# Kernel tuning notes

Measured on AMD Instinct MI355X. Metric: run time of the kernel, lower is better.

The kernel has to match this reference:

```python
import jax, jax.numpy as jnp
import numpy as np

B, C, H, W = 16, 512, 64, 64
SCALE = 8
CQK = C // SCALE  # 64
EPS = 1e-6


def setup_inputs() -> dict:
    key = jax.random.key(0)
    ks = jax.random.split(key, 8)
    x = jax.random.normal(ks[0], (B, C, H, W), dtype=jnp.float32)
    # 1x1 conv weights stored as [out_ch, in_ch] (kernel_size=1)
    Wq = jax.random.normal(ks[1], (CQK, C), dtype=jnp.float32) * 0.02
    bq = jnp.zeros((CQK,), dtype=jnp.float32)
    Wk = jax.random.normal(ks[2], (CQK, C), dtype=jnp.float32) * 0.02
    bk = jnp.zeros((CQK,), dtype=jnp.float32)
    Wv = jax.random.normal(ks[3], (C, C), dtype=jnp.float32) * 0.02
    bv = jnp.zeros((C,), dtype=jnp.float32)
    # gamma is initialized to 0 in the module; use a nonzero value so the
    # output is non-trivial for kernel correctness checks.
    gamma = jax.random.normal(ks[4], (1,), dtype=jnp.float32)
    return {"x": x, "Wq": Wq, "bq": bq, "Wk": Wk, "bk": bk,
            "Wv": Wv, "bv": bv, "gamma": gamma}


def _l2norm_ch(t):
    # normalize over the channel axis (dim=-2), matching torch.norm(p=2, dim=-2)
    nrm = jnp.sqrt(jnp.sum(t * t, axis=-2, keepdims=True))
    return t / jnp.maximum(nrm, EPS)


def reference(x, Wq, bq, Wk, bk, Wv, bv, gamma):
    b, c, h, w = x.shape
    n = h * w
    xf = x.reshape(b, c, n)                                   # [B,C,N]
    # 1x1 convs == channel matmuls
    Q = jnp.einsum('oc,bcn->bon', Wq, xf) + bq[None, :, None]  # [B,cqk,N]
    K = jnp.einsum('oc,bcn->bon', Wk, xf) + bk[None, :, None]  # [B,cqk,N]
    V = jnp.einsum('oc,bcn->bon', Wv, xf) + bv[None, :, None]  # [B,C,N]
    Qn = _l2norm_ch(Q).transpose(0, 2, 1)                      # [B,N,cqk]
    Kn = _l2norm_ch(K)                                         # [B,cqk,N]
    # Taylor-softmax surrogate denominator
    denom = n + jnp.einsum('bnc,bc->bn', Qn, Kn.sum(axis=-1))  # [B,N]
    tailor = 1.0 / jnp.maximum(denom, 1e-6)                    # [B,N]
    # KtV accumulation: [B,cqk,C]
    matrix = jnp.einsum('bmn,bcn->bmc', Kn, V)
    value_sum = jnp.sum(V, axis=-1)[:, :, None]                # [B,C,1] -> broadcast
    matrix_sum = value_sum + jnp.einsum('bnm,bmc->bcn', Qn, matrix)  # [B,C,N]
    weight_value = matrix_sum * tailor[:, None, :]             # [B,C,N]
    out = gamma * weight_value.reshape(b, c, h, w)
    return jnp.nan_to_num(out, nan=0.0, posinf=1.0, neginf=-1.0)
```

## Files before the change

kernel.cpp:

```cpp
#include <hip/hip_runtime.h>


typedef __attribute__((ext_vector_type(8))) short short8_t;
typedef __attribute__((ext_vector_type(4))) float f32x4;

__device__ __forceinline__ unsigned short f2bf(float f) {
  union { float f; unsigned u; } v; v.f = f;
  unsigned r = v.u + 0x7FFFu + ((v.u >> 16) & 1u);
  return (unsigned short)(r >> 16);
}
__device__ __forceinline__ float bf2f(unsigned short h) {
  union { unsigned u; float f; } v; v.u = ((unsigned)h) << 16;
  return v.f;
}

#define MFMA(a, b, c) __builtin_amdgcn_mfma_f32_16x16x32_bf16((a), (b), (c), 0, 0, 0)

__global__ void k_prep(const float* __restrict__ Wq, const float* __restrict__ Wk,
                       unsigned short* __restrict__ Wqk) {
  int idx = blockIdx.x * 256 + threadIdx.x;
  int o = idx >> 9, c = idx & 511;
  float v = (o < 64) ? Wq[o * 512 + c] : Wk[(o - 64) * 512 + c];
  Wqk[idx] = f2bf(v);
}

__launch_bounds__(256, 2)
__global__ void k_qk(const float* __restrict__ x, const unsigned short* __restrict__ Wqk,
                     const float* __restrict__ bq, const float* __restrict__ bk,
                     unsigned short* __restrict__ QnT, unsigned short* __restrict__ KnG,
                     float* __restrict__ Ksum) {
  __shared__ __align__(16) unsigned char smem[77312];
  unsigned short* SAb[2] = {(unsigned short*)(smem + 0),
                            (unsigned short*)(smem + 18432)};
  unsigned short* SBb[2] = {(unsigned short*)(smem + 36864),
                            (unsigned short*)(smem + 55296)};
  unsigned short* EQ = (unsigned short*)(smem + 0);
  unsigned short* EK = (unsigned short*)(smem + 18432);
  float* ssq   = (float*)(smem + 73728);
  float* invq  = (float*)(smem + 75776);
  float* invk  = (float*)(smem + 76288);
  float* biasL = (float*)(smem + 76800);

  const int t = threadIdx.x;
  const int lane = t & 63, w = t >> 6;
  const int l15 = lane & 15, quad = lane >> 4;
  const int nt = blockIdx.x, b = blockIdx.y;
  const int n0 = nt * 128;
  const float* xb = x + (size_t)b * 512 * 4096;

  if (t < 128) biasL[t] = (t < 64) ? bq[t] : bk[t - 64];

  f32x4 acc[2][8];
#pragma unroll
  for (int i = 0; i < 2; ++i)
#pragma unroll
    for (int j = 0; j < 8; ++j) acc[i][j] = (f32x4){0.f, 0.f, 0.f, 0.f};

  const int nB = t & 127;
  const int cgB = t >> 7;
  const float* bsrc0 = xb + (size_t)(cgB * 32) * 4096 + n0 + nB;

  short8_t apre[4];
  float bpre[32];

#define QK_LOADA(kc_) do {                                                     \
    const int c0_ = (kc_) * 64;                                                \
    _Pragma("unroll")                                                          \
    for (int p = 0; p < 4; ++p) {                                              \
      int gid = t + p * 256; int o_ = gid >> 3, cg = gid & 7;                  \
      apre[p] = *(const short8_t*)(Wqk + o_ * 512 + c0_ + cg * 8);             \
    } } while (0)

#define QK_LOADB(kc_) do {                                                     \
    const float* s_ = bsrc0 + (size_t)(kc_) * 64 * 4096;                       \
    _Pragma("unroll")                                                          \
    for (int i = 0; i < 32; ++i) bpre[i] = s_[(size_t)i * 4096];               \
    } while (0)

#define QK_STORE(pb) do {                                                      \
    unsigned short* SAp = SAb[pb]; unsigned short* SBp = SBb[pb];              \
    _Pragma("unroll")                                                          \
    for (int p = 0; p < 4; ++p) {                                              \
      int gid = t + p * 256; int o_ = gid >> 3, cg = gid & 7;                  \
      *(short8_t*)(SAp + o_ * 72 + cg * 8) = apre[p];                          \
    }                                                                          \
    _Pragma("unroll")                                                          \
    for (int j = 0; j < 4; ++j) {                                              \
      short8_t v_;                                                             \
      _Pragma("unroll")                                                        \
      for (int e = 0; e < 8; ++e) v_[e] = (short)f2bf(bpre[j * 8 + e]);        \
      *(short8_t*)(SBp + nB * 72 + cgB * 32 + j * 8) = v_;                     \
    } } while (0)

#define QK_MM(pb) do {                                                         \
    const unsigned short* SAp = SAb[pb]; const unsigned short* SBp = SBb[pb];  \
    _Pragma("unroll")                                                          \
    for (int s = 0; s < 2; ++s) {                                              \
      short8_t a0 = *(const short8_t*)(SAp + (w * 32 + l15) * 72 + s * 32 + quad * 8);      \
      short8_t a1 = *(const short8_t*)(SAp + (w * 32 + 16 + l15) * 72 + s * 32 + quad * 8); \
      _Pragma("unroll")                                                        \
      for (int tc = 0; tc < 8; ++tc) {                                         \
        short8_t bf_ = *(const short8_t*)(SBp + (tc * 16 + l15) * 72 + s * 32 + quad * 8);  \
        acc[0][tc] = MFMA(a0, bf_, acc[0][tc]);                                \
        acc[1][tc] = MFMA(a1, bf_, acc[1][tc]);                                \
      } } } while (0)

  QK_LOADA(0); QK_LOADB(0);
#pragma unroll
  for (int kc = 0; kc < 8; ++kc) {
    const int pb = kc & 1;
    QK_STORE(pb);
    if (kc < 7) { QK_LOADA(kc + 1); QK_LOADB(kc + 1); }
    __syncthreads();
    QK_MM(pb);
  }
  __syncthreads();

#pragma unroll
  for (int trl = 0; trl < 2; ++trl)
#pragma unroll
    for (int reg = 0; reg < 4; ++reg) {
      int o = w * 32 + trl * 16 + quad * 4 + reg;
      float bias = biasL[o];
#pragma unroll
      for (int tc = 0; tc < 8; ++tc) acc[trl][tc][reg] += bias;
    }

#pragma unroll
  for (int tc = 0; tc < 8; ++tc) {
    float v = 0.f;
#pragma unroll
    for (int trl = 0; trl < 2; ++trl)
#pragma unroll
      for (int reg = 0; reg < 4; ++reg) {
        float q = acc[trl][tc][reg];
        v += q * q;
      }
    v += __shfl_xor(v, 16);
    v += __shfl_xor(v, 32);
    if (quad == 0) ssq[w * 128 + tc * 16 + l15] = v;
  }
  __syncthreads();
  if (t < 128) {
    float qs = ssq[t] + ssq[128 + t];
    float ks = ssq[256 + t] + ssq[384 + t];
    invq[t] = 1.0f / fmaxf(sqrtf(qs), 1e-6f);
    invk[t] = 1.0f / fmaxf(sqrtf(ks), 1e-6f);
  }
  __syncthreads();

  if (w < 2) {
#pragma unroll
    for (int trl = 0; trl < 2; ++trl)
#pragma unroll
      for (int tc = 0; tc < 8; ++tc) {
        int n = tc * 16 + l15;
        float inv = invq[n];
#pragma unroll
        for (int reg = 0; reg < 4; ++reg) {
          int o = w * 32 + trl * 16 + quad * 4 + reg;
          EQ[n * 72 + o] = f2bf(acc[trl][tc][reg] * inv);
        }
      }
  } else {
#pragma unroll
    for (int trl = 0; trl < 2; ++trl)
#pragma unroll
      for (int reg = 0; reg < 4; ++reg) {
        int m = (w - 2) * 32 + trl * 16 + quad * 4 + reg;
        float p = 0.f;
#pragma unroll
        for (int tc = 0; tc < 8; ++tc) {
          int n = tc * 16 + l15;
          float val = acc[trl][tc][reg] * invk[n];
          EK[m * 136 + n] = f2bf(val);
          p += val;
        }
        p += __shfl_xor(p, 1);
        p += __shfl_xor(p, 2);
        p += __shfl_xor(p, 4);
        p += __shfl_xor(p, 8);
        if (l15 == 0) atomicAdd(Ksum + b * 64 + m, p);
      }
  }
  __syncthreads();

  unsigned short* qdst = QnT + ((size_t)b * 4096 + n0) * 64;
#pragma unroll
  for (int p = 0; p < 4; ++p) {
    int idx = t + p * 256;
    int row = idx >> 3, seg = idx & 7;
    *(short8_t*)(qdst + row * 64 + seg * 8) = *(const short8_t*)(EQ + row * 72 + seg * 8);
  }
  unsigned short* kdst = KnG + (size_t)b * 64 * 4096 + n0;
#pragma unroll
  for (int p = 0; p < 4; ++p) {
    int idx = t + p * 256;
    int row = idx >> 4, seg = idx & 15;
    *(short8_t*)(kdst + (size_t)row * 4096 + seg * 8) =
        *(const short8_t*)(EK + row * 136 + seg * 8);
  }
#undef QK_LOADA
#undef QK_LOADB
#undef QK_STORE
#undef QK_MM
}

__launch_bounds__(256, 2)
__global__ void k_t(const float* __restrict__ x, const unsigned short* __restrict__ KnG,
                    float* __restrict__ T, float* __restrict__ xsum) {
  __shared__ __align__(16) unsigned char smem[55296];
  unsigned short* SAb[2] = {(unsigned short*)(smem + 0),
                            (unsigned short*)(smem + 9216)};
  unsigned short* SBb[2] = {(unsigned short*)(smem + 18432),
                            (unsigned short*)(smem + 36864)};
  const int t = threadIdx.x;
  const int lane = t & 63, w = t >> 6;
  const int l15 = lane & 15, quad = lane >> 4;
  const int ns = blockIdx.x, ct = blockIdx.y, b = blockIdx.z;
  const int c0 = ct * 128;
  const float* xb = x + (size_t)b * 512 * 4096;
  const unsigned short* Knb = KnG + (size_t)b * 64 * 4096 + ns * 512;

  f32x4 acc[4][2];
#pragma unroll
  for (int i = 0; i < 4; ++i)
#pragma unroll
    for (int j = 0; j < 2; ++j) acc[i][j] = (f32x4){0.f, 0.f, 0.f, 0.f};

  const int row = t >> 1, half = t & 1;
  float xs = 0.f;
  const float* bbase = xb + (size_t)(c0 + row) * 4096 + ns * 512 + half * 32;

  short8_t apre[2];
  f32x4 bpre[8];

#define T_LOADA(ch_) do {                                                      \
    _Pragma("unroll")                                                          \
    for (int p = 0; p < 2; ++p) {                                              \
      int gid = t + p * 256; int m_ = gid >> 3, cg = gid & 7;                  \
      apre[p] = *(const short8_t*)(Knb + (size_t)m_ * 4096 + (ch_) * 64 + cg * 8); \
    } } while (0)

#define T_LOADB(ch_) do {                                                      \
    const float* s_ = bbase + (ch_) * 64;                                      \
    _Pragma("unroll")                                                          \
    for (int q = 0; q < 8; ++q) bpre[q] = *(const f32x4*)(s_ + q * 4);         \
    } while (0)

#define T_STORE(pb) do {                                                       \
    unsigned short* SAp = SAb[pb]; unsigned short* SBp = SBb[pb];              \
    _Pragma("unroll")                                                          \
    for (int p = 0; p < 2; ++p) {                                              \
      int gid = t + p * 256; int m_ = gid >> 3, cg = gid & 7;                  \
      *(short8_t*)(SAp + m_ * 72 + cg * 8) = apre[p];                          \
    }                                                                          \
    _Pragma("unroll")                                                          \
    for (int j = 0; j < 4; ++j) {                                              \
      short8_t v_;                                                             \
      _Pragma("unroll")                                                        \
      for (int e = 0; e < 4; ++e) {                                            \
        float f0 = bpre[j * 2][e], f1 = bpre[j * 2 + 1][e];                    \
        xs += f0 + f1;                                                         \
        v_[e] = (short)f2bf(f0); v_[4 + e] = (short)f2bf(f1);                  \
      }                                                                        \
      *(short8_t*)(SBp + row * 72 + half * 32 + j * 8) = v_;                   \
    } } while (0)

#define T_MM(pb) do {                                                          \
    const unsigned short* SAp = SAb[pb]; const unsigned short* SBp = SBb[pb];  \
    _Pragma("unroll")                                                          \
    for (int s = 0; s < 2; ++s) {                                              \
      short8_t af[4];                                                          \
      _Pragma("unroll")                                                        \
      for (int tm = 0; tm < 4; ++tm)                                           \
        af[tm] = *(const short8_t*)(SAp + (tm * 16 + l15) * 72 + s * 32 + quad * 8); \
      _Pragma("unroll")                                                        \
      for (int tcl = 0; tcl < 2; ++tcl) {                                      \
        short8_t bf_ = *(const short8_t*)(SBp + (w * 32 + tcl * 16 + l15) * 72 + s * 32 + quad * 8); \
        _Pragma("unroll")                                                      \
        for (int tm = 0; tm < 4; ++tm) acc[tm][tcl] = MFMA(af[tm], bf_, acc[tm][tcl]); \
      } } } while (0)

  T_LOADA(0); T_LOADB(0);
#pragma unroll
  for (int ch = 0; ch < 8; ++ch) {
    const int pb = ch & 1;
    T_STORE(pb);
    if (ch < 7) { T_LOADA(ch + 1); T_LOADB(ch + 1); }
    __syncthreads();
    T_MM(pb);
  }

  xs += __shfl_xor(xs, 1);
  if (half == 0) atomicAdd(xsum + b * 512 + c0 + row, xs);
#pragma unroll
  for (int tm = 0; tm < 4; ++tm)
#pragma unroll
    for (int tcl = 0; tcl < 2; ++tcl)
#pragma unroll
      for (int reg = 0; reg < 4; ++reg) {
        int m = tm * 16 + quad * 4 + reg;
        int c = c0 + w * 32 + tcl * 16 + l15;
        atomicAdd(T + ((size_t)b * 64 + m) * 512 + c, acc[tm][tcl][reg]);
      }
#undef T_LOADA
#undef T_LOADB
#undef T_STORE
#undef T_MM
}

__launch_bounds__(256, 2)
__global__ void k_mat(const float* __restrict__ T, const float* __restrict__ Wv,
                      const float* __restrict__ bv, const float* __restrict__ xsum,
                      const float* __restrict__ Ksum,
                      unsigned short* __restrict__ matT, float* __restrict__ Vsum) {
  __shared__ __align__(16) unsigned char smem[27136];
  float* ST = (float*)smem;
  float* SW = (float*)(smem + 17408);
  float* SV = (float*)(smem + 26112);
  const int t = threadIdx.x;
  const int cb = blockIdx.x, b = blockIdx.y;
  const int c0 = cb * 32;
  const int m = t >> 2, cs = t & 3;
  float acc[8] = {0.f, 0.f, 0.f, 0.f, 0.f, 0.f, 0.f, 0.f};

  for (int kc = 0; kc < 8; ++kc) {
    __syncthreads();
#pragma unroll
    for (int p = 0; p < 4; ++p) {
      int idx = t + p * 256;
      int row = idx >> 4, f4 = idx & 15;
      *(f32x4*)(ST + row * 68 + f4 * 4) =
          *(const f32x4*)(T + ((size_t)b * 64 + row) * 512 + kc * 64 + f4 * 4);
    }
#pragma unroll
    for (int p = 0; p < 2; ++p) {
      int idx = t + p * 256;
      int row = idx >> 4, f4 = idx & 15;
      *(f32x4*)(SW + row * 68 + f4 * 4) =
          *(const f32x4*)(Wv + (size_t)(c0 + row) * 512 + kc * 64 + f4 * 4);
    }
    __syncthreads();
    for (int kk = 0; kk < 64; ++kk) {
      float tv = ST[m * 68 + kk];
#pragma unroll
      for (int j = 0; j < 8; ++j) acc[j] += tv * SW[(cs + j * 4) * 68 + kk];
    }
  }
  float ks = Ksum[b * 64 + m];
#pragma unroll
  for (int j = 0; j < 8; ++j) {
    int c = c0 + cs + j * 4;
    float mv = acc[j] + bv[c] * ks;
    matT[((size_t)b * 512 + c) * 64 + m] = f2bf(mv);
  }
  {
    int cc = t >> 3, kp = t & 7;
    const float* wr = Wv + (size_t)(c0 + cc) * 512 + kp * 64;
    const float* xr = xsum + b * 512 + kp * 64;
    float s = 0.f;
    for (int i = 0; i < 64; ++i) s += wr[i] * xr[i];
    SV[cc * 8 + kp] = s;
  }
  __syncthreads();
  if (t < 32) {
    float s = 0.f;
#pragma unroll
    for (int i = 0; i < 8; ++i) s += SV[t * 8 + i];
    int c = c0 + t;
    Vsum[b * 512 + c] = s + 4096.0f * bv[c];
  }
}

__launch_bounds__(256, 2)
__global__ void k_out(const unsigned short* __restrict__ QnT,
                      const unsigned short* __restrict__ matT,
                      const float* __restrict__ Ksum, const float* __restrict__ Vsum,
                      const float* __restrict__ gamma, float* __restrict__ out) {
  __shared__ __align__(16) unsigned char smem[38144];
  unsigned short* SA = (unsigned short*)smem;
  unsigned short* SB = (unsigned short*)(smem + 18432);
  float* Ksl  = (float*)(smem + 36864);
  float* tail = (float*)(smem + 37120);
  float* vs   = (float*)(smem + 37632);
  const int t = threadIdx.x;
  const int lane = t & 63, w = t >> 6;
  const int l15 = lane & 15, quad = lane >> 4;
  const int nt = blockIdx.x, ct = blockIdx.y, b = blockIdx.z;
  const int n0 = nt * 128, c0 = ct * 128;

  const unsigned short* asrc = matT + ((size_t)b * 512 + c0) * 64;
  const unsigned short* bsrc = QnT + ((size_t)b * 4096 + n0) * 64;
#pragma unroll
  for (int p = 0; p < 4; ++p) {
    int idx = t + p * 256;
    int row = idx >> 3, seg = idx & 7;
    *(short8_t*)(SA + row * 72 + seg * 8) = *(const short8_t*)(asrc + row * 64 + seg * 8);
    *(short8_t*)(SB + row * 72 + seg * 8) = *(const short8_t*)(bsrc + row * 64 + seg * 8);
  }
  if (t < 64) Ksl[t] = Ksum[b * 64 + t];
  if (t >= 128) vs[t - 128] = Vsum[b * 512 + c0 + (t - 128)];
  __syncthreads();
  if (t < 128) {
    float d = 0.f;
#pragma unroll
    for (int mm = 0; mm < 64; ++mm) d += bf2f(SB[t * 72 + mm]) * Ksl[mm];
    tail[t] = 1.0f / fmaxf(4096.0f + d, 1e-6f);
  }

  f32x4 acc[2][8];
#pragma unroll
  for (int i = 0; i < 2; ++i)
#pragma unroll
    for (int j = 0; j < 8; ++j) acc[i][j] = (f32x4){0.f, 0.f, 0.f, 0.f};

#pragma unroll
  for (int s = 0; s < 2; ++s) {
    short8_t a0 = *(const short8_t*)(SA + (w * 32 + l15) * 72 + s * 32 + quad * 8);
    short8_t a1 = *(const short8_t*)(SA + (w * 32 + 16 + l15) * 72 + s * 32 + quad * 8);
#pragma unroll
    for (int tc = 0; tc < 8; ++tc) {
      short8_t bfr = *(const short8_t*)(SB + (tc * 16 + l15) * 72 + s * 32 + quad * 8);
      acc[0][tc] = MFMA(a0, bfr, acc[0][tc]);
      acc[1][tc] = MFMA(a1, bfr, acc[1][tc]);
    }
  }
  __syncthreads();
  const float g = gamma[0];
  float* ob = out + (size_t)b * 512 * 4096;
#pragma unroll
  for (int trl = 0; trl < 2; ++trl)
#pragma unroll
    for (int tc = 0; tc < 8; ++tc) {
      int n = tc * 16 + l15;
      float tl = tail[n] * g;
#pragma unroll
      for (int reg = 0; reg < 4; ++reg) {
        int cl = w * 32 + trl * 16 + quad * 4 + reg;
        float val = tl * (vs[cl] + acc[trl][tc][reg]);
        ob[(size_t)(c0 + cl) * 4096 + n0 + n] = val;
      }
    }
}

extern "C" void kernel_launch(void* const* d_in, const int* in_sizes, int n_in,
                              void* d_out, int out_size, void* d_ws, size_t ws_size,
                              hipStream_t stream) {
  const float* x     = (const float*)d_in[0];
  const float* Wq    = (const float*)d_in[1];
  const float* bq    = (const float*)d_in[2];
  const float* Wk    = (const float*)d_in[3];
  const float* bk    = (const float*)d_in[4];
  const float* Wv    = (const float*)d_in[5];
  const float* bv    = (const float*)d_in[6];
  const float* gamma = (const float*)d_in[7];
  float* out = (float*)d_out;
  char* ws = (char*)d_ws;

  float* T    = (float*)(ws + 0);
  float* xsum = (float*)(ws + 2097152);
  float* Ksum = (float*)(ws + 2129920);
  float* Vsum = (float*)(ws + 2134016);
  unsigned short* Wqk  = (unsigned short*)(ws + 2166784);
  unsigned short* matT = (unsigned short*)(ws + 2297856);
  unsigned short* QnT  = (unsigned short*)(ws + 3346432);
  unsigned short* Kn   = (unsigned short*)(ws + 11735040);

  hipMemsetAsync(ws, 0, 2134016, stream);
  k_prep<<<256, 256, 0, stream>>>(Wq, Wk, Wqk);
  k_qk<<<dim3(32, 16), 256, 0, stream>>>(x, Wqk, bq, bk, QnT, Kn, Ksum);
  k_t<<<dim3(8, 4, 16), 256, 0, stream>>>(x, Kn, T, xsum);
  k_mat<<<dim3(16, 16), 256, 0, stream>>>(T, Wv, bv, xsum, Ksum, matT, Vsum);
  k_out<<<dim3(32, 4, 16), 256, 0, stream>>>(QnT, matT, Ksum, Vsum, gamma, out);
}
```

Baseline: 322.5 us.

## Replace atomic T accumulation with per-split partial buffers and a reduce kernel

k_t now writes each N-split's partial T tile to its own slice of a new partial buffer with plain stores instead of float atomicAdd, and a new k_red kernel sums the eight partials into T. The memset shrinks to only the xsum/Ksum/Vsum region. Separately, k_mat is re-tiled so each thread computes a 2x4 output block with float4 LDS reads and writes packed bf16 pairs. This removes atomic contention and most of the memset, at the cost of 16 MB of extra partial traffic and one more kernel launch.

```diff
diff --git a/kernel.cpp b/kernel.cpp
--- a/kernel.cpp
+++ b/kernel.cpp
@@ -208,7 +208,7 @@
 
 __launch_bounds__(256, 2)
 __global__ void k_t(const float* __restrict__ x, const unsigned short* __restrict__ KnG,
-                    float* __restrict__ T, float* __restrict__ xsum) {
+                    float* __restrict__ Tpart, float* __restrict__ xsum) {
   __shared__ __align__(16) unsigned char smem[55296];
   unsigned short* SAb[2] = {(unsigned short*)(smem + 0),
                             (unsigned short*)(smem + 9216)};
@@ -294,6 +294,7 @@
 
   xs += __shfl_xor(xs, 1);
   if (half == 0) atomicAdd(xsum + b * 512 + c0 + row, xs);
+  float* Tp = Tpart + ((size_t)(ns * 16 + b) * 64) * 512;
 #pragma unroll
   for (int tm = 0; tm < 4; ++tm)
 #pragma unroll
@@ -302,12 +303,21 @@
       for (int reg = 0; reg < 4; ++reg) {
         int m = tm * 16 + quad * 4 + reg;
         int c = c0 + w * 32 + tcl * 16 + l15;
-        atomicAdd(T + ((size_t)b * 64 + m) * 512 + c, acc[tm][tcl][reg]);
+        Tp[(size_t)m * 512 + c] = acc[tm][tcl][reg];
       }
 #undef T_LOADA
 #undef T_LOADB
 #undef T_STORE
 #undef T_MM
+}
+
+__global__ void k_red(const float* __restrict__ Tpart, float* __restrict__ T) {
+  size_t idx = (size_t)blockIdx.x * 256 + threadIdx.x;
+  const f32x4* p = (const f32x4*)Tpart + idx;
+  f32x4 s = p[0];
+#pragma unroll
+  for (int ns = 1; ns < 8; ++ns) s += p[(size_t)ns * 131072];
+  ((f32x4*)T)[idx] = s;
 }
 
 __launch_bounds__(256, 2)
@@ -322,8 +332,9 @@
   const int t = threadIdx.x;
   const int cb = blockIdx.x, b = blockIdx.y;
   const int c0 = cb * 32;
-  const int m = t >> 2, cs = t & 3;
-  float acc[8] = {0.f, 0.f, 0.f, 0.f, 0.f, 0.f, 0.f, 0.f};
+  const int mp = t >> 3, cs = t & 7;
+  f32x4 acc0 = (f32x4){0.f, 0.f, 0.f, 0.f};
+  f32x4 acc1 = (f32x4){0.f, 0.f, 0.f, 0.f};
 
   for (int kc = 0; kc < 8; ++kc) {
     __syncthreads();
@@ -342,18 +353,30 @@
           *(const f32x4*)(Wv + (size_t)(c0 + row) * 512 + kc * 64 + f4 * 4);
     }
     __syncthreads();
-    for (int kk = 0; kk < 64; ++kk) {
-      float tv = ST[m * 68 + kk];
-#pragma unroll
-      for (int j = 0; j < 8; ++j) acc[j] += tv * SW[(cs + j * 4) * 68 + kk];
+#pragma unroll 4
+    for (int kk = 0; kk < 64; kk += 4) {
+      f32x4 t0 = *(const f32x4*)(ST + (2 * mp) * 68 + kk);
+      f32x4 t1 = *(const f32x4*)(ST + (2 * mp + 1) * 68 + kk);
+#pragma unroll
+      for (int j = 0; j < 4; ++j) {
+        f32x4 wv = *(const f32x4*)(SW + (cs + j * 8) * 68 + kk);
+#pragma unroll
+        for (int e = 0; e < 4; ++e) {
+          acc0[j] = fmaf(t0[e], wv[e], acc0[j]);
+          acc1[j] = fmaf(t1[e], wv[e], acc1[j]);
+        }
+      }
     }
   }
-  float ks = Ksum[b * 64 + m];
-#pragma unroll
-  for (int j = 0; j < 8; ++j) {
-    int c = c0 + cs + j * 4;
-    float mv = acc[j] + bv[c] * ks;
-    matT[((size_t)b * 512 + c) * 64 + m] = f2bf(mv);
+  float ks0 = Ksum[b * 64 + 2 * mp];
+  float ks1 = Ksum[b * 64 + 2 * mp + 1];
+#pragma unroll
+  for (int j = 0; j < 4; ++j) {
+    int c = c0 + cs + j * 8;
+    float bvc = bv[c];
+    unsigned lo = f2bf(acc0[j] + bvc * ks0);
+    unsigned hi = f2bf(acc1[j] + bvc * ks1);
+    *(unsigned*)(matT + ((size_t)b * 512 + c) * 64 + 2 * mp) = lo | (hi << 16);
   }
   {
     int cc = t >> 3, kp = t & 7;
@@ -458,19 +481,21 @@
   float* out = (float*)d_out;
   char* ws = (char*)d_ws;
 
-  float* T    = (float*)(ws + 0);
-  float* xsum = (float*)(ws + 2097152);
-  float* Ksum = (float*)(ws + 2129920);
-  float* Vsum = (float*)(ws + 2134016);
-  unsigned short* Wqk  = (unsigned short*)(ws + 2166784);
-  unsigned short* matT = (unsigned short*)(ws + 2297856);
-  unsigned short* QnT  = (unsigned short*)(ws + 3346432);
-  unsigned short* Kn   = (unsigned short*)(ws + 11735040);
-
-  hipMemsetAsync(ws, 0, 2134016, stream);
+  float* Tpart = (float*)(ws + 0);
+  float* T     = (float*)(ws + 16777216);
+  float* xsum  = (float*)(ws + 18874368);
+  float* Ksum  = (float*)(ws + 18907136);
+  float* Vsum  = (float*)(ws + 18911232);
+  unsigned short* Wqk  = (unsigned short*)(ws + 18944000);
+  unsigned short* matT = (unsigned short*)(ws + 19075072);
+  unsigned short* QnT  = (unsigned short*)(ws + 20123648);
+  unsigned short* Kn   = (unsigned short*)(ws + 28512256);
+
+  hipMemsetAsync(ws + 18874368, 0, 36864, stream);
   k_prep<<<256, 256, 0, stream>>>(Wq, Wk, Wqk);
   k_qk<<<dim3(32, 16), 256, 0, stream>>>(x, Wqk, bq, bk, QnT, Kn, Ksum);
-  k_t<<<dim3(8, 4, 16), 256, 0, stream>>>(x, Kn, T, xsum);
+  k_t<<<dim3(8, 4, 16), 256, 0, stream>>>(x, Kn, Tpart, xsum);
+  k_red<<<512, 256, 0, stream>>>(Tpart, T);
   k_mat<<<dim3(16, 16), 256, 0, stream>>>(T, Wv, bv, xsum, Ksum, matT, Vsum);
   k_out<<<dim3(32, 4, 16), 256, 0, stream>>>(QnT, matT, Ksum, Vsum, gamma, out);
 }
```

New measurement: 323.1 us. Within noise of the previous version (+0.2%).
